# Kernel optimization log

Measured on AMD Instinct MI355X. Metric: run time of the kernel, lower is better.

The kernel has to match this reference:

```python
import jax, jax.numpy as jnp
import numpy as np

N, E = 50000, 800000
IN_C, H_C, OUT_C, HEADS = 64, 32, 32, 8


def setup_inputs() -> dict:
    key = jax.random.key(0)
    ks = jax.random.split(key, 16)
    def glorot(k, shape):
        fan_in = shape[-1]
        return jax.random.normal(k, shape, dtype=jnp.float32) / jnp.sqrt(jnp.float32(fan_in))
    inp = {
        'x': jax.random.normal(ks[0], (N, IN_C), dtype=jnp.float32),
        'edge_index': jax.random.randint(ks[1], (2, E), 0, N, dtype=jnp.int64),
        # layer 1: in_c -> h_c, heads
        'W1l': glorot(ks[2], (HEADS * H_C, IN_C)),
        'b1l': jnp.zeros((HEADS * H_C,), jnp.float32),
        'W1r': glorot(ks[3], (HEADS * H_C, IN_C)),
        'b1r': jnp.zeros((HEADS * H_C,), jnp.float32),
        'att1': glorot(ks[4], (HEADS, H_C)),
        'bias1': jnp.zeros((H_C,), jnp.float32),
        # layer 2: h_c -> out_c, heads
        'W2l': glorot(ks[5], (HEADS * OUT_C, H_C)),
        'b2l': jnp.zeros((HEADS * OUT_C,), jnp.float32),
        'W2r': glorot(ks[6], (HEADS * OUT_C, H_C)),
        'b2r': jnp.zeros((HEADS * OUT_C,), jnp.float32),
        'att2': glorot(ks[7], (HEADS, OUT_C)),
        'bias2': jnp.zeros((OUT_C,), jnp.float32),
    }
    return inp


def _gatv2_layer(x, src, dst, valid, Wl, bl, Wr, br, att, bias):
    # PyG GATv2Conv (share_weights=False, concat=False): message j->i uses
    # e = att . leaky_relu(lin_l(x_j) + lin_r(x_i), 0.2); softmax over dst; agg lin_l(x_j).
    n = x.shape[0]
    heads, c = att.shape
    xl = (x @ Wl.T + bl).reshape(n, heads, c)
    xr = (x @ Wr.T + br).reshape(n, heads, c)
    m = jax.nn.leaky_relu(xl[src] + xr[dst], negative_slope=0.2)  # [Etot,H,C]
    score = jnp.einsum('ehc,hc->eh', m, att)                      # [Etot,H]
    score = jnp.where(valid[:, None], score, -jnp.inf)
    smax = jax.ops.segment_max(score, dst, num_segments=n)        # [N,H]
    a = jnp.where(valid[:, None], jnp.exp(score - smax[dst]), 0.0)
    denom = jax.ops.segment_sum(a, dst, num_segments=n)
    a = a / jnp.maximum(denom[dst], 1e-16)
    out = jax.ops.segment_sum(a[..., None] * xl[src], dst, num_segments=n)  # [N,H,C]
    return out.mean(axis=1) + bias


def reference(x, edge_index, W1l, b1l, W1r, b1r, att1, bias1,
              W2l, b2l, W2r, b2r, att2, bias2):
    n = x.shape[0]
    src0, dst0 = edge_index[0], edge_index[1]
    # PyG removes existing self loops then adds fresh ones: mask originals,
    # append one self loop per node (keeps static shapes).
    loop = jnp.arange(n, dtype=src0.dtype)
    src = jnp.concatenate([src0, loop])
    dst = jnp.concatenate([dst0, loop])
    valid = jnp.concatenate([src0 != dst0, jnp.ones((n,), bool)])
    h = _gatv2_layer(x, src, dst, valid, W1l, b1l, W1r, b1r, att1, bias1)
    h = jax.nn.leaky_relu(h, negative_slope=0.01)  # nn.LeakyReLU default
    out = _gatv2_layer(h, src, dst, valid, W2l, b2l, W2r, b2r, att2, bias2)
    return out
```

## Files before the change

kernel.cpp:

```cpp
#include <hip/hip_runtime.h>
#include <math.h>

#define HEADS 8
#define CDIM 32
#define ODIM 256
#define BKT_SHIFT 7
#define CHUNK 4096
#define CAP 4096

typedef _Float16 h2 __attribute__((ext_vector_type(2)));
typedef _Float16 h4 __attribute__((ext_vector_type(4)));
typedef _Float16 h8 __attribute__((ext_vector_type(8)));
typedef float f32x4 __attribute__((ext_vector_type(4)));
typedef unsigned long long u64;
union H4 { h4 v; h2 p[2]; u64 u; };

#if __has_builtin(__builtin_amdgcn_fdot2)
#define FDOT2(a,b,c) __builtin_amdgcn_fdot2((a),(b),(c),false)
#else
static __device__ __forceinline__ float fdot2_sw(h2 a, h2 b, float c){
  return fmaf((float)a.x, (float)b.x, fmaf((float)a.y, (float)b.y, c));
}
#define FDOT2(a,b,c) fdot2_sw((a),(b),(c))
#endif

__device__ __forceinline__ float lrelu(float v, float s){ return fmaxf(v, s*v); }


__global__ __launch_bounds__(512) void csr_offs_kernel(
    int* __restrict__ hist, int* __restrict__ btotal, int NB, int B){
  __shared__ int s[512];
  int b = blockIdx.x, t = threadIdx.x;
  int v = (t < NB) ? hist[t*B + b] : 0;
  s[t] = v;
  __syncthreads();
  for (int off=1; off<512; off<<=1){
    int u = (t >= off) ? s[t-off] : 0;
    __syncthreads(); s[t] += u; __syncthreads();
  }
  int excl = s[t] - v;
  if (t < NB) hist[t*B + b] = excl;
  if (t == NB-1) btotal[b] = excl + v;
}

__global__ __launch_bounds__(512) void csr_scatter_kernel(
    const int* __restrict__ src, const int* __restrict__ dst,
    const int* __restrict__ rank, const int* __restrict__ offs,
    int* __restrict__ bpack, int e, int B){
  int t = threadIdx.x, k = blockIdx.x;
  int base_i = k*CHUNK;
#pragma unroll
  for (int j = 0; j < CHUNK/512; ++j){
    int i = base_i + j*512 + t;
    if (i < e){
      int r = rank[i];
      if (r >= 0){
        int d = dst[i], sv = src[i];
        int b = d >> BKT_SHIFT;
        int pos = b*CAP + offs[k*B + b] + r;
        bpack[pos] = (sv << BKT_SHIFT) | (d & 127);
      }
    }
  }
}

__global__ __launch_bounds__(512) void csr_sort_kernel(
    const int* __restrict__ bpack, const int* __restrict__ btotal,
    int* __restrict__ csr, int* __restrict__ ind_beg, int* __restrict__ ind_end,
    int n, int B){
  __shared__ int lh[128], cur[128], ss[128];
  int b = blockIdx.x, t = threadIdx.x;
  int beg = b*CAP;
  int cnt = btotal[b]; if (cnt > CAP) cnt = CAP;
  if (t < 128) lh[t] = 0;
  __syncthreads();
  for (int j = t; j < cnt; j += 512)
    atomicAdd(&lh[bpack[beg+j] & 127], 1);
  __syncthreads();
  int v = (t < 128) ? lh[t] : 0;
  if (t < 128) ss[t] = v;
  __syncthreads();
  for (int off=1; off<128; off<<=1){
    int u = (t >= off && t < 128) ? ss[t-off] : 0;
    __syncthreads();
    if (t < 128) ss[t] += u;
    __syncthreads();
  }
  if (t < 128){
    int excl = ss[t] - v;
    cur[t] = excl;
    int node = (b << BKT_SHIFT) + t;
    if (node < n){ ind_beg[node] = beg + excl; ind_end[node] = beg + excl + v; }
  }
  __syncthreads();
  for (int j = t; j < cnt; j += 512){
    int p = bpack[beg + j];
    int lpos = atomicAdd(&cur[p & 127], 1);
    csr[beg + lpos] = p >> BKT_SHIFT;
  }
}

template<int K, bool FUSE_AUX, bool W_F32>
__global__ __launch_bounds__(512) void gemm_mfma(const float* __restrict__ X,
    const void* __restrict__ Wl, const float* __restrict__ bl,
    const void* __restrict__ Wr, const float* __restrict__ br,
    _Float16* __restrict__ outl, _Float16* __restrict__ outr, int n,
    const int* __restrict__ src, const int* __restrict__ dst,
    int* __restrict__ rank, int* __restrict__ hist, int e, int B,
    const float* __restrict__ W2l, const float* __restrict__ W2r,
    _Float16* __restrict__ w2lh, _Float16* __restrict__ w2rh){
  if (FUSE_AUX && blockIdx.y == 1){
    int k = blockIdx.x;
    int NB = (e + CHUNK-1)/CHUNK;
    int t = threadIdx.x;
    if (k < NB){
      __shared__ int lh[512];
      lh[t] = 0;
      __syncthreads();
      int base_i = k*CHUNK;
#pragma unroll
      for (int j = 0; j < CHUNK/512; ++j){
        int i = base_i + j*512 + t;
        if (i < e){
          int s = src[i], d = dst[i];
          int r = -1;
          if (s != d) r = atomicAdd(&lh[d>>BKT_SHIFT], 1);
          rank[i] = r;
        }
      }
      __syncthreads();
      for (int b = t; b < B; b += 512) hist[k*B + b] = lh[b];
    } else if (k < NB + 8){
      int i = ((k - NB)*512 + t)*4;
      const float* s; _Float16* d; int off;
      if (i < 8192){ s = W2l; d = w2lh; off = i; }
      else         { s = W2r; d = w2rh; off = i - 8192; }
      float4 v = *(const float4*)(s + off);
      *(h4*)(d + off) = (h4){(_Float16)v.x, (_Float16)v.y, (_Float16)v.z, (_Float16)v.w};
    }
    return;
  }
  const int KP = K + 8;
  __shared__ __align__(16) _Float16 Xs[64*(K+8)];
  int t = threadIdx.x;
  int n0 = blockIdx.x*64;

  for (int idx = t; idx < 64*(K/4); idx += 512){
    int row = idx/(K/4), c = (idx%(K/4))*4;
    int node = n0 + row; if (node >= n) node = n-1;
    f32x4 xv = __builtin_nontemporal_load((const f32x4*)(X + (size_t)node*K + c));
    *(h4*)(Xs + row*KP + c) = (h4){(_Float16)xv[0], (_Float16)xv[1],
                                   (_Float16)xv[2], (_Float16)xv[3]};
  }
  __syncthreads();

  int wave = t >> 6, lane = t & 63;
  int co = wave*64;
  const void* W   = (co < 256) ? Wl : Wr;
  const float* Bv = (co < 256) ? bl : br;
  _Float16* outp  = (co < 256) ? outl : outr;
  int lco = co & 255;
  int lr = lane & 15, lg = lane >> 4;

  f32x4 acc[4][4];
#pragma unroll
  for (int c = 0; c < 4; ++c)
#pragma unroll
    for (int m = 0; m < 4; ++m) acc[c][m] = (f32x4){0.f, 0.f, 0.f, 0.f};

#pragma unroll
  for (int ks = 0; ks < K/32; ++ks){
    int k0 = ks*32 + lg*8;
    h8 a[4], b[4];
#pragma unroll
    for (int c = 0; c < 4; ++c){
      if (W_F32){
        const float* wp = (const float*)W + (size_t)(lco + c*16 + lr)*K + k0;
        float4 w0 = *(const float4*)(wp);
        float4 w1 = *(const float4*)(wp + 4);
        a[c] = (h8){(_Float16)w0.x,(_Float16)w0.y,(_Float16)w0.z,(_Float16)w0.w,
                    (_Float16)w1.x,(_Float16)w1.y,(_Float16)w1.z,(_Float16)w1.w};
      } else {
        a[c] = *(const h8*)((const _Float16*)W + (size_t)(lco + c*16 + lr)*K + k0);
      }
    }
#pragma unroll
    for (int m = 0; m < 4; ++m)
      b[m] = *(const h8*)(Xs + (m*16 + lr)*KP + k0);
#pragma unroll
    for (int c = 0; c < 4; ++c)
#pragma unroll
      for (int m = 0; m < 4; ++m)
        acc[c][m] = __builtin_amdgcn_mfma_f32_16x16x32_f16(a[c], b[m], acc[c][m], 0, 0, 0);
  }

#pragma unroll
  for (int c = 0; c < 4; ++c){
    int ch = lco + c*16 + lg*4;
    float4 bb = *(const float4*)(Bv + ch);
#pragma unroll
    for (int m = 0; m < 4; ++m){
      int node = n0 + m*16 + lr;
      if (node < n){
        h4 o = {(_Float16)(acc[c][m][0] + bb.x), (_Float16)(acc[c][m][1] + bb.y),
                (_Float16)(acc[c][m][2] + bb.z), (_Float16)(acc[c][m][3] + bb.w)};
        *(h4*)(outp + (size_t)node*ODIM + ch) = o;
      }
    }
  }
}

__global__ __launch_bounds__(256) void edge_kernel(
    const _Float16* __restrict__ xl, const _Float16* __restrict__ xr,
    const float* __restrict__ att, const float* __restrict__ bias,
    const int* __restrict__ ind_beg, const int* __restrict__ ind_end,
    const int* __restrict__ csr_src,
    float* __restrict__ out, int n, int act)
{
  int wid = blockIdx.x*4 + (threadIdx.x >> 6);
  if (wid >= n) return;
  int lane = threadIdx.x & 63;
  const float LOG2E = 1.44269504088896341f;

  float4 attf = *(const float4*)(att + 4*lane);
  h2 at0 = (h2){(_Float16)(attf.x*LOG2E), (_Float16)(attf.y*LOG2E)};
  h2 at1 = (h2){(_Float16)(attf.z*LOG2E), (_Float16)(attf.w*LOG2E)};
  const h2 c02 = {(_Float16)0.2f, (_Float16)0.2f};

  H4 xrh; xrh.u = __builtin_nontemporal_load((const u64*)(xr + (size_t)wid*ODIM + 4*lane));
  H4 self; self.v = *(const h4*)(xl + (size_t)wid*ODIM + 4*lane);

  auto score = [&](const H4& c)->float{
    h2 t0 = c.p[0] + xrh.p[0];
    h2 t1 = c.p[1] + xrh.p[1];
    h2 q0 = __builtin_elementwise_max(t0, t0 * c02);
    h2 q1 = __builtin_elementwise_max(t1, t1 * c02);
    float d = FDOT2(q0, at0, FDOT2(q1, at1, 0.f));
    d += __shfl_xor(d, 1);
    d += __shfl_xor(d, 2);
    d += __shfl_xor(d, 4);
    return d;
  };

  float w0 = exp2f(score(self));
  float denom = w0;
  float4 acc;
  acc.x = w0 * (float)self.v.x;
  acc.y = w0 * (float)self.v.y;
  acc.z = w0 * (float)self.v.z;
  acc.w = w0 * (float)self.v.w;

  int beg = __builtin_amdgcn_readfirstlane(ind_beg[wid]);
  int end = __builtin_amdgcn_readfirstlane(ind_end[wid]);
  int cnt = end - beg;

#define GATHER(j) (*(const h4*)(xl + (size_t)((unsigned)__shfl(sidx,(j)))*ODIM + 4*lane))
  for (int cb = 0; cb < cnt; cb += 64){
    int ccnt = min(cnt - cb, 64);
    int sidx = (lane < ccnt) ? __builtin_nontemporal_load(csr_src + beg + cb + lane) : 0;
    H4 r0, r1, r2, r3;
    r0.v = (h4){}; r1.v = (h4){}; r2.v = (h4){}; r3.v = (h4){};
    if (ccnt > 0) r0.v = GATHER(0);
    if (ccnt > 1) r1.v = GATHER(1);
    if (ccnt > 2) r2.v = GATHER(2);
    if (ccnt > 3) r3.v = GATHER(3);
#pragma unroll 2
    for (int k = 0; k < ccnt; k += 2){
      H4 e0 = r0, e1 = r1;
      r0 = r2; r1 = r3;
      if (k+4 < ccnt) r2.v = GATHER(k+4);
      if (k+5 < ccnt) r3.v = GATHER(k+5);
      float s0 = score(e0);
      float s1 = score(e1);
      float pe0 = exp2f(s0);
      float pe1 = (k+1 < ccnt) ? exp2f(s1) : 0.f;
      denom += pe0 + pe1;
      acc.x = fmaf(pe0, (float)e0.v.x, fmaf(pe1, (float)e1.v.x, acc.x));
      acc.y = fmaf(pe0, (float)e0.v.y, fmaf(pe1, (float)e1.v.y, acc.y));
      acc.z = fmaf(pe0, (float)e0.v.z, fmaf(pe1, (float)e1.v.z, acc.z));
      acc.w = fmaf(pe0, (float)e0.v.w, fmaf(pe1, (float)e1.v.w, acc.w));
    }
  }
#undef GATHER

  float inv = 1.f/denom;
  float vx = acc.x*inv, vy = acc.y*inv, vz = acc.z*inv, vw = acc.w*inv;
  vx += __shfl_xor(vx, 8);  vx += __shfl_xor(vx, 16);  vx += __shfl_xor(vx, 32);
  vy += __shfl_xor(vy, 8);  vy += __shfl_xor(vy, 16);  vy += __shfl_xor(vy, 32);
  vz += __shfl_xor(vz, 8);  vz += __shfl_xor(vz, 16);  vz += __shfl_xor(vz, 32);
  vw += __shfl_xor(vw, 8);  vw += __shfl_xor(vw, 16);  vw += __shfl_xor(vw, 32);
  if (lane < 8){
    float4 bv = *(const float4*)(bias + 4*lane);
    float ox = vx*0.125f + bv.x;
    float oy = vy*0.125f + bv.y;
    float oz = vz*0.125f + bv.z;
    float ow = vw*0.125f + bv.w;
    if (act){
      ox = lrelu(ox, 0.01f); oy = lrelu(oy, 0.01f);
      oz = lrelu(oz, 0.01f); ow = lrelu(ow, 0.01f);
    }
    f32x4 ov = {ox, oy, oz, ow};
    __builtin_nontemporal_store(ov, (f32x4*)(out + (size_t)wid*CDIM + 4*lane));
  }
}

extern "C" void kernel_launch(void* const* d_in, const int* in_sizes, int n_in,
                              void* d_out, int out_size, void* d_ws, size_t ws_size,
                              hipStream_t stream){
  (void)n_in; (void)out_size; (void)ws_size;
  const float* x    = (const float*)d_in[0];
  const int*   ei   = (const int*)d_in[1];
  const float* W1l  = (const float*)d_in[2];
  const float* b1l  = (const float*)d_in[3];
  const float* W1r  = (const float*)d_in[4];
  const float* b1r  = (const float*)d_in[5];
  const float* att1 = (const float*)d_in[6];
  const float* bias1= (const float*)d_in[7];
  const float* W2l  = (const float*)d_in[8];
  const float* b2l  = (const float*)d_in[9];
  const float* W2r  = (const float*)d_in[10];
  const float* b2r  = (const float*)d_in[11];
  const float* att2 = (const float*)d_in[12];
  const float* bias2= (const float*)d_in[13];
  int n = in_sizes[0] / 64;
  int e = in_sizes[1] / 2;
  const int* srcp = ei;
  const int* dstp = ei + e;

  char* ws = (char*)d_ws;
  size_t off = 0;
  auto alloc = [&](size_t bytes)->char*{
    char* p = ws + off; off += (bytes + 255) & ~(size_t)255; return p;
  };
  _Float16* xl  = (_Float16*)alloc((size_t)n*ODIM*2);
  _Float16* xr  = (_Float16*)alloc((size_t)n*ODIM*2);
  float* h      = (float*)alloc((size_t)n*CDIM*4);
  int*   ind_beg = (int*)alloc((size_t)n*4);
  int*   ind_end = (int*)alloc((size_t)n*4);
  int*   rank   = (int*)alloc((size_t)e*4);

  int NB = (e + CHUNK-1) / CHUNK;
  int B  = (n + 127) >> 7;
  int*   csr    = (int*)alloc((size_t)B*CAP*4);
  int*   bpack  = (int*)alloc((size_t)B*CAP*4);
  _Float16* w2lh = (_Float16*)alloc((size_t)ODIM*32*2);
  _Float16* w2rh = (_Float16*)alloc((size_t)ODIM*32*2);
  int*   hist   = (int*)alloc((size_t)NB*B*4);
  int*   btotal = (int*)alloc((size_t)B*4);

  int nt64 = (n + 63) / 64;

  gemm_mfma<64,true,true><<<dim3(nt64,2), 512, 0, stream>>>(
      x, W1l, b1l, W1r, b1r, xl, xr, n, srcp, dstp, rank, hist, e, B,
      W2l, W2r, w2lh, w2rh);
  csr_offs_kernel<<<B, 512, 0, stream>>>(hist, btotal, NB, B);
  csr_scatter_kernel<<<NB, 512, 0, stream>>>(srcp, dstp, rank, hist, bpack, e, B);
  csr_sort_kernel<<<B, 512, 0, stream>>>(bpack, btotal, csr, ind_beg, ind_end, n, B);

  edge_kernel<<<(n+3)/4, 256, 0, stream>>>(xl, xr, att1, bias1, ind_beg, ind_end, csr, h, n, 1);
  gemm_mfma<32,false,false><<<dim3(nt64,1), 512, 0, stream>>>(
      h, w2lh, b2l, w2rh, b2r, xl, xr, n, nullptr, nullptr, nullptr, nullptr, 0, 0,
      nullptr, nullptr, nullptr, nullptr);
  edge_kernel<<<(n+3)/4, 256, 0, stream>>>(xl, xr, att2, bias2, ind_beg, ind_end, csr, (float*)d_out, n, 0);
}
```

Baseline: 304.6 us.

## Process two node tiles per GEMM block with register-prefetched second tile

The MFMA GEMM grid is fixed at 512 blocks, and each block handles up to two 64-node tiles. The weight fragments and bias are loaded into registers once and reused for both tiles. The second tile's X rows are prefetched into registers while the first tile is computed, then staged into a second shared-memory buffer. This spreads the weight load and launch cost over more work and overlaps global loads with MFMA compute, at the cost of higher register and shared-memory use and fewer resident blocks.

```diff
diff --git a/kernel.cpp b/kernel.cpp
--- a/kernel.cpp
+++ b/kernel.cpp
@@ -7,6 +7,7 @@
 #define BKT_SHIFT 7
 #define CHUNK 4096
 #define CAP 4096
+#define GB 512
 
 typedef _Float16 h2 __attribute__((ext_vector_type(2)));
 typedef _Float16 h4 __attribute__((ext_vector_type(4)));
@@ -141,16 +142,33 @@
     return;
   }
   const int KP = K + 8;
-  __shared__ __align__(16) _Float16 Xs[64*(K+8)];
+  const int NKS = K/32;
+  const int NLD = (64*(K/4))/512;
+  __shared__ __align__(16) _Float16 Xs[2][64*(K+8)];
   int t = threadIdx.x;
-  int n0 = blockIdx.x*64;
-
-  for (int idx = t; idx < 64*(K/4); idx += 512){
+  int nt = (n + 63) >> 6;
+  int tb0 = blockIdx.x;
+  int tb1 = blockIdx.x + GB;
+  bool has1 = (tb1 < nt);
+
+#pragma unroll
+  for (int j = 0; j < NLD; ++j){
+    int idx = t + j*512;
     int row = idx/(K/4), c = (idx%(K/4))*4;
-    int node = n0 + row; if (node >= n) node = n-1;
+    int node = tb0*64 + row; if (node >= n) node = n-1;
     f32x4 xv = __builtin_nontemporal_load((const f32x4*)(X + (size_t)node*K + c));
-    *(h4*)(Xs + row*KP + c) = (h4){(_Float16)xv[0], (_Float16)xv[1],
-                                   (_Float16)xv[2], (_Float16)xv[3]};
+    *(h4*)(Xs[0] + row*KP + c) = (h4){(_Float16)xv[0], (_Float16)xv[1],
+                                      (_Float16)xv[2], (_Float16)xv[3]};
+  }
+  f32x4 p1[NLD];
+  if (has1){
+#pragma unroll
+    for (int j = 0; j < NLD; ++j){
+      int idx = t + j*512;
+      int row = idx/(K/4), c = (idx%(K/4))*4;
+      int node = tb1*64 + row; if (node >= n) node = n-1;
+      p1[j] = __builtin_nontemporal_load((const f32x4*)(X + (size_t)node*K + c));
+    }
   }
   __syncthreads();
 
@@ -162,51 +180,74 @@
   int lco = co & 255;
   int lr = lane & 15, lg = lane >> 4;
 
-  f32x4 acc[4][4];
-#pragma unroll
-  for (int c = 0; c < 4; ++c)
-#pragma unroll
-    for (int m = 0; m < 4; ++m) acc[c][m] = (f32x4){0.f, 0.f, 0.f, 0.f};
-
-#pragma unroll
-  for (int ks = 0; ks < K/32; ++ks){
+  h8 wf[NKS][4];
+#pragma unroll
+  for (int ks = 0; ks < NKS; ++ks){
     int k0 = ks*32 + lg*8;
-    h8 a[4], b[4];
 #pragma unroll
     for (int c = 0; c < 4; ++c){
       if (W_F32){
         const float* wp = (const float*)W + (size_t)(lco + c*16 + lr)*K + k0;
         float4 w0 = *(const float4*)(wp);
         float4 w1 = *(const float4*)(wp + 4);
-        a[c] = (h8){(_Float16)w0.x,(_Float16)w0.y,(_Float16)w0.z,(_Float16)w0.w,
-                    (_Float16)w1.x,(_Float16)w1.y,(_Float16)w1.z,(_Float16)w1.w};
+        wf[ks][c] = (h8){(_Float16)w0.x,(_Float16)w0.y,(_Float16)w0.z,(_Float16)w0.w,
+                         (_Float16)w1.x,(_Float16)w1.y,(_Float16)w1.z,(_Float16)w1.w};
       } else {
-        a[c] = *(const h8*)((const _Float16*)W + (size_t)(lco + c*16 + lr)*K + k0);
+        wf[ks][c] = *(const h8*)((const _Float16*)W + (size_t)(lco + c*16 + lr)*K + k0);
       }
     }
-#pragma unroll
-    for (int m = 0; m < 4; ++m)
-      b[m] = *(const h8*)(Xs + (m*16 + lr)*KP + k0);
+  }
+
+  float4 bb[4];
+#pragma unroll
+  for (int c = 0; c < 4; ++c) bb[c] = *(const float4*)(Bv + lco + c*16 + lg*4);
+
+  auto compute = [&](const _Float16* buf, int n0){
+    f32x4 acc[4][4];
 #pragma unroll
     for (int c = 0; c < 4; ++c)
 #pragma unroll
+      for (int m = 0; m < 4; ++m) acc[c][m] = (f32x4){0.f, 0.f, 0.f, 0.f};
+#pragma unroll
+    for (int ks = 0; ks < NKS; ++ks){
+      int k0 = ks*32 + lg*8;
+      h8 b[4];
+#pragma unroll
       for (int m = 0; m < 4; ++m)
-        acc[c][m] = __builtin_amdgcn_mfma_f32_16x16x32_f16(a[c], b[m], acc[c][m], 0, 0, 0);
-  }
-
-#pragma unroll
-  for (int c = 0; c < 4; ++c){
-    int ch = lco + c*16 + lg*4;
-    float4 bb = *(const float4*)(Bv + ch);
-#pragma unroll
-    for (int m = 0; m < 4; ++m){
-      int node = n0 + m*16 + lr;
-      if (node < n){
-        h4 o = {(_Float16)(acc[c][m][0] + bb.x), (_Float16)(acc[c][m][1] + bb.y),
-                (_Float16)(acc[c][m][2] + bb.z), (_Float16)(acc[c][m][3] + bb.w)};
-        *(h4*)(outp + (size_t)node*ODIM + ch) = o;
+        b[m] = *(const h8*)(buf + (m*16 + lr)*KP + k0);
+#pragma unroll
+      for (int c = 0; c < 4; ++c)
+#pragma unroll
+        for (int m = 0; m < 4; ++m)
+          acc[c][m] = __builtin_amdgcn_mfma_f32_16x16x32_f16(wf[ks][c], b[m], acc[c][m], 0, 0, 0);
+    }
+#pragma unroll
+    for (int c = 0; c < 4; ++c){
+      int ch = lco + c*16 + lg*4;
+#pragma unroll
+      for (int m = 0; m < 4; ++m){
+        int node = n0 + m*16 + lr;
+        if (node < n){
+          h4 o = {(_Float16)(acc[c][m][0] + bb[c].x), (_Float16)(acc[c][m][1] + bb[c].y),
+                  (_Float16)(acc[c][m][2] + bb[c].z), (_Float16)(acc[c][m][3] + bb[c].w)};
+          *(h4*)(outp + (size_t)node*ODIM + ch) = o;
+        }
       }
     }
+  };
+
+  compute(Xs[0], tb0*64);
+
+  if (has1){
+#pragma unroll
+    for (int j = 0; j < NLD; ++j){
+      int idx = t + j*512;
+      int row = idx/(K/4), c = (idx%(K/4))*4;
+      *(h4*)(Xs[1] + row*KP + c) = (h4){(_Float16)p1[j][0], (_Float16)p1[j][1],
+                                        (_Float16)p1[j][2], (_Float16)p1[j][3]};
+    }
+    __syncthreads();
+    compute(Xs[1], tb1*64);
   }
 }
 
@@ -348,9 +389,7 @@
   int*   hist   = (int*)alloc((size_t)NB*B*4);
   int*   btotal = (int*)alloc((size_t)B*4);
 
-  int nt64 = (n + 63) / 64;
-
-  gemm_mfma<64,true,true><<<dim3(nt64,2), 512, 0, stream>>>(
+  gemm_mfma<64,true,true><<<dim3(GB,2), 512, 0, stream>>>(
       x, W1l, b1l, W1r, b1r, xl, xr, n, srcp, dstp, rank, hist, e, B,
       W2l, W2r, w2lh, w2rh);
   csr_offs_kernel<<<B, 512, 0, stream>>>(hist, btotal, NB, B);
@@ -358,7 +397,7 @@
   csr_sort_kernel<<<B, 512, 0, stream>>>(bpack, btotal, csr, ind_beg, ind_end, n, B);
 
   edge_kernel<<<(n+3)/4, 256, 0, stream>>>(xl, xr, att1, bias1, ind_beg, ind_end, csr, h, n, 1);
-  gemm_mfma<32,false,false><<<dim3(nt64,1), 512, 0, stream>>>(
+  gemm_mfma<32,false,false><<<dim3(GB,1), 512, 0, stream>>>(
       h, w2lh, b2l, w2rh, b2r, xl, xr, n, nullptr, nullptr, nullptr, nullptr, 0, 0,
       nullptr, nullptr, nullptr, nullptr);
   edge_kernel<<<(n+3)/4, 256, 0, stream>>>(xl, xr, att2, bias2, ind_beg, ind_end, csr, (float*)d_out, n, 0);
```

New measurement: 288.1 us. 5.4% less time.
